# Kernel optimization log

Hardware: AMD Instinct MI355X
Metric: run time of the kernel (lower is better)

## Reference

```python
import jax, jax.numpy as jnp
import numpy as np

N, HW, A, G, C = 8, 4096, 9, 64, 80


def setup_inputs() -> dict:
    key = jax.random.key(0)
    k1, k2, k3, k4, k5, k6 = jax.random.split(key, 6)
    pred_boxes = jax.random.uniform(k1, (N, HW, A, 4), dtype=jnp.float32)  # (x, y, w, h) in [0,1)
    pred_o = jax.random.uniform(k2, (N, HW, A), dtype=jnp.float32)
    pred_scores = jax.random.normal(k3, (N, HW, A, C), dtype=jnp.float32)
    # valid xyxy ground-truth boxes with positive width/height
    xy = jax.random.uniform(k4, (N, G, 2), dtype=jnp.float32) * 0.7
    wh = 0.05 + jax.random.uniform(k5, (N, G, 2), dtype=jnp.float32) * 0.25
    gt_boxes = jnp.concatenate([xy, xy + wh], axis=-1)
    gt_labels = jax.random.randint(k6, (N, G), 0, C)
    return dict(pred_boxes=pred_boxes, pred_o=pred_o, pred_scores=pred_scores,
                gt_boxes=gt_boxes, gt_labels=gt_labels)


def _box_iou(b1, b2):
    # b1 [P,4], b2 [G,4] in xyxy -> [P,G]; same math as torchvision.ops.box_iou
    a1 = (b1[:, 2] - b1[:, 0]) * (b1[:, 3] - b1[:, 1])
    a2 = (b2[:, 2] - b2[:, 0]) * (b2[:, 3] - b2[:, 1])
    lt = jnp.maximum(b1[:, None, :2], b2[None, :, :2])
    rb = jnp.minimum(b1[:, None, 2:], b2[None, :, 2:])
    wh = jnp.clip(rb - lt, 0.0)
    inter = wh[..., 0] * wh[..., 1]
    return inter / (a1[:, None] + a2[None, :] - inter)


def _per_image(pb, po, ps, gb, gl):
    # pb [HW,A,4] already converted to xyxy, po [HW,A], ps [HW,A,C], gb [G,4], gl [G]
    iou = _box_iou(pb.reshape(-1, 4), gb).reshape(HW, A, G)
    cell_sel = iou.max(axis=(1, 2)) > 0.0                  # [HW] cells with any GT overlap
    anchor_sel = jnp.argmax(iou.max(axis=2), axis=1)       # [HW] best anchor per cell
    hw = jnp.arange(HW)
    sel_boxes = pb[hw, anchor_sel]                         # [HW,4]
    sel_o = po[hw, anchor_sel]                             # [HW]
    sel_scores = ps[hw, anchor_sel]                        # [HW,C]
    iou_sel = iou[hw, anchor_sel]                          # [HW,G]
    best_iou = iou_sel.max(axis=1)
    best_gt = jnp.argmax(iou_sel, axis=1)
    gt_b = gb[best_gt]                                     # [HW,4]
    gt_l = gl[best_gt]                                     # [HW]
    m = cell_sel.astype(pb.dtype)
    obj = jnp.sum(m * (sel_o - best_iou) ** 2)
    bbox = jnp.sum(m[:, None] * (sel_boxes[:, :2] - gt_b[:, :2]) ** 2)
    bbox += jnp.sum(m[:, None] * (jnp.sqrt(sel_boxes[:, 2:]) - jnp.sqrt(gt_b[:, 2:])) ** 2)
    ce = -jnp.take_along_axis(jax.nn.log_softmax(sel_scores, axis=-1), gt_l[:, None], axis=1)[:, 0]
    clf = jnp.sum(m * ce)
    # empty cells: penalize max objectness over anchors
    obj += 0.5 * jnp.sum((1.0 - m) * po.max(axis=1) ** 2)
    return obj, bbox, clf


def reference(pred_boxes, pred_o, pred_scores, gt_boxes, gt_labels):
    # (x,y,w,h) -> (x,y,x+w,y+h), as done in-place in the torch code
    pb = jnp.concatenate([pred_boxes[..., :2], pred_boxes[..., 2:] + pred_boxes[..., :2]], axis=-1)
    obj, bbox, clf = jax.vmap(_per_image)(pb, pred_o, pred_scores, gt_boxes, gt_labels)
    return jnp.stack([obj.sum(), bbox.sum(), clf.sum()])
```

## Files before the change

### kernel.cpp

```cpp
#include <hip/hip_runtime.h>
#include <math.h>

#define NIMG 8
#define HWC  4096
#define AA   9
#define GG   64
#define CC   80
#define CPB  64
#define BT   (CPB * AA)
#define NSLOT 32

__global__ __launch_bounds__(BT) void yolo_main(
    const float* __restrict__ pred_boxes,
    const float* __restrict__ pred_o,
    const float* __restrict__ pred_scores,
    const float* __restrict__ gt_boxes,
    const int*   __restrict__ gt_labels,
    float*       __restrict__ part)
{
    __shared__ float4 sbox[GG];
    __shared__ float  sarea[GG];
    __shared__ float  ssqx[GG];
    __shared__ float  ssqy[GG];
    __shared__ int    slab[GG];
    __shared__ float  Li[BT];
    __shared__ float  Ls[BT];
    __shared__ int    Lg[BT];
    __shared__ float4 Lbox[BT];
    __shared__ float  Lpo[BT];
    __shared__ int    Lsel[CPB];
    __shared__ int    Llbl[CPB];

    const int tid = threadIdx.x;
    const int n   = blockIdx.y;
    const int hw0 = blockIdx.x * CPB;

    if (tid < GG) {
        float4 gb = ((const float4*)gt_boxes)[n * GG + tid];
        sbox[tid]  = gb;
        sarea[tid] = (gb.z - gb.x) * (gb.w - gb.y);
        ssqx[tid]  = sqrtf(gb.z);
        ssqy[tid]  = sqrtf(gb.w);
        slab[tid]  = gt_labels[n * GG + tid];
    }
    __syncthreads();

    const int c    = tid / AA;
    const int a    = tid - c * AA;
    const int cell = hw0 + c;
    const int pidx = (n * HWC + cell) * AA + a;

    const float4 pb = ((const float4*)pred_boxes)[pidx];
    const float  po = pred_o[pidx];
    const float x1 = pb.x, y1 = pb.y;
    const float x2 = pb.x + pb.z, y2 = pb.y + pb.w;
    const float a1 = (x2 - x1) * (y2 - y1);

    float bi = -1.0f, bsv = 1.0f; int bg = 0;
    #pragma unroll 8
    for (int g = 0; g < GG; ++g) {
        float4 gb = sbox[g];
        float s  = a1 + sarea[g];
        float ix = fminf(x2, gb.z) - fmaxf(x1, gb.x);
        float iy = fminf(y2, gb.w) - fmaxf(y1, gb.y);
        float inter = fmaxf(ix, 0.0f) * fmaxf(iy, 0.0f);
        if (inter * bsv > bi * s) { bi = inter; bsv = s; bg = g; }
    }
    Li[tid]  = bi;
    Ls[tid]  = bsv;
    Lg[tid]  = bg;
    Lbox[tid] = make_float4(x1, y1, x2, y2);
    Lpo[tid] = po;
    __syncthreads();

    if (tid < CPB) {
        const int cc = tid;
        float bi2 = -1.0f, bs2 = 1.0f; int ba = 0;
        float pomax = -1e30f;
        #pragma unroll
        for (int aa2 = 0; aa2 < AA; ++aa2) {
            float ii = Li[cc * AA + aa2];
            float ss = Ls[cc * AA + aa2];
            if (ii * bs2 > bi2 * ss) { bi2 = ii; bs2 = ss; ba = aa2; }
            pomax = fmaxf(pomax, Lpo[cc * AA + aa2]);
        }
        float objv, bboxv = 0.0f;
        int selbase = -1, lbl = 0;
        if (bi2 > 0.0f) {
            float biou = bi2 / (bs2 - bi2);
            float4 sb  = Lbox[cc * AA + ba];
            int    g   = Lg[cc * AA + ba];
            float4 gb  = sbox[g];
            float  so  = Lpo[cc * AA + ba];
            float d = so - biou;
            objv = d * d;
            float dx = sb.x - gb.x, dy = sb.y - gb.y;
            float dz = sqrtf(sb.z) - ssqx[g];
            float dw = sqrtf(sb.w) - ssqy[g];
            bboxv = dx*dx + dy*dy + dz*dz + dw*dw;
            selbase = ((n * HWC + hw0 + cc) * AA + ba) * CC;
            lbl = slab[g];
        } else {
            objv = 0.5f * pomax * pomax;
        }
        Lsel[cc] = selbase;
        Llbl[cc] = lbl;
        float ov = objv, bv = bboxv;
        #pragma unroll
        for (int msk = 1; msk < 64; msk <<= 1) {
            ov += __shfl_xor(ov, msk);
            bv += __shfl_xor(bv, msk);
        }
        if (tid == 0) {
            int slot = blockIdx.x & (NSLOT - 1);
            atomicAdd(&part[0 * NSLOT + slot], ov);
            atomicAdd(&part[1 * NSLOT + slot], bv);
        }
    }
    __syncthreads();

    {
        const int sb = Lsel[c];
        float esum = 0.0f, selv = 0.0f;
        if (sb >= 0) {
            const int lbl = Llbl[c];
            #pragma unroll
            for (int i = 0; i < AA; ++i) {
                int e = a + AA * i;
                if (e < CC) {
                    float v = pred_scores[sb + e];
                    esum += __expf(v);
                    if (e == lbl) selv = v;
                }
            }
        }
        Li[tid] = esum;
        Ls[tid] = selv;
    }
    __syncthreads();

    if (tid < CPB) {
        float clfv = 0.0f;
        if (Lsel[tid] >= 0) {
            float S = 0.0f, sel = 0.0f;
            #pragma unroll
            for (int aa2 = 0; aa2 < AA; ++aa2) {
                S   += Li[tid * AA + aa2];
                sel += Ls[tid * AA + aa2];
            }
            clfv = __logf(S) - sel;
        }
        #pragma unroll
        for (int msk = 1; msk < 64; msk <<= 1) clfv += __shfl_xor(clfv, msk);
        if (tid == 0) {
            int slot = blockIdx.x & (NSLOT - 1);
            atomicAdd(&part[2 * NSLOT + slot], clfv);
        }
    }
}

__global__ void yolo_final(const float* __restrict__ part, float* __restrict__ out)
{
    int t = threadIdx.x;
    float v = (t < 3 * NSLOT) ? part[t] : 0.0f;
    #pragma unroll
    for (int msk = 1; msk < NSLOT; msk <<= 1) v += __shfl_xor(v, msk, NSLOT);
    if (t < 3 * NSLOT && (t & (NSLOT - 1)) == 0) out[t / NSLOT] = v;
}

extern "C" void kernel_launch(void* const* d_in, const int* in_sizes, int n_in,
                              void* d_out, int out_size, void* d_ws, size_t ws_size,
                              hipStream_t stream)
{
    const float* pred_boxes  = (const float*)d_in[0];
    const float* pred_o      = (const float*)d_in[1];
    const float* pred_scores = (const float*)d_in[2];
    const float* gt_boxes    = (const float*)d_in[3];
    const int*   gt_labels   = (const int*)d_in[4];
    float* part = (float*)d_ws;

    hipMemsetAsync(d_ws, 0, 3 * NSLOT * sizeof(float), stream);
    dim3 grid(HWC / CPB, NIMG);
    yolo_main<<<grid, BT, 0, stream>>>(pred_boxes, pred_o, pred_scores,
                                       gt_boxes, gt_labels, part);
    yolo_final<<<1, 128, 0, stream>>>(part, (float*)d_out);
}
```

Before: 146.6 us.

## Replace atomics and memset with per-block partials, vectorize score loads

Each block writes its objectness, bbox and classification partial sums to a dedicated workspace slot instead of atomically accumulating into 32 slots. This removes the memset launch and the atomic contention. The final kernel reduces all 512 partials with a 512-thread block. The IoU loop now reads GT boxes straight from global memory (cache-resident) with inline area computation, dropping the first block barrier, and class scores are loaded as float4.

```diff
diff --git a/kernel.cpp b/kernel.cpp
--- a/kernel.cpp
+++ b/kernel.cpp
@@ -8,7 +8,7 @@
 #define CC   80
 #define CPB  64
 #define BT   (CPB * AA)
-#define NSLOT 32
+#define NBLK (NIMG * (HWC / CPB))
 
 __global__ __launch_bounds__(BT) void yolo_main(
     const float* __restrict__ pred_boxes,
@@ -19,7 +19,6 @@
     float*       __restrict__ part)
 {
     __shared__ float4 sbox[GG];
-    __shared__ float  sarea[GG];
     __shared__ float  ssqx[GG];
     __shared__ float  ssqy[GG];
     __shared__ int    slab[GG];
@@ -37,13 +36,11 @@
 
     if (tid < GG) {
         float4 gb = ((const float4*)gt_boxes)[n * GG + tid];
-        sbox[tid]  = gb;
-        sarea[tid] = (gb.z - gb.x) * (gb.w - gb.y);
-        ssqx[tid]  = sqrtf(gb.z);
-        ssqy[tid]  = sqrtf(gb.w);
-        slab[tid]  = gt_labels[n * GG + tid];
-    }
-    __syncthreads();
+        sbox[tid] = gb;
+        ssqx[tid] = sqrtf(gb.z);
+        ssqy[tid] = sqrtf(gb.w);
+        slab[tid] = gt_labels[n * GG + tid];
+    }
 
     const int c    = tid / AA;
     const int a    = tid - c * AA;
@@ -56,15 +53,21 @@
     const float x2 = pb.x + pb.z, y2 = pb.y + pb.w;
     const float a1 = (x2 - x1) * (y2 - y1);
 
+    const float4* __restrict__ gbp = (const float4*)gt_boxes + n * GG;
+
     float bi = -1.0f, bsv = 1.0f; int bg = 0;
-    #pragma unroll 8
-    for (int g = 0; g < GG; ++g) {
-        float4 gb = sbox[g];
-        float s  = a1 + sarea[g];
-        float ix = fminf(x2, gb.z) - fmaxf(x1, gb.x);
-        float iy = fminf(y2, gb.w) - fmaxf(y1, gb.y);
-        float inter = fmaxf(ix, 0.0f) * fmaxf(iy, 0.0f);
-        if (inter * bsv > bi * s) { bi = inter; bsv = s; bg = g; }
+    #pragma unroll 1
+    for (int g0 = 0; g0 < GG; g0 += 8) {
+        #pragma unroll
+        for (int k = 0; k < 8; ++k) {
+            const float4 gb = gbp[g0 + k];
+            const float area = (gb.z - gb.x) * (gb.w - gb.y);
+            const float s  = a1 + area;
+            const float ix = fminf(x2, gb.z) - fmaxf(x1, gb.x);
+            const float iy = fminf(y2, gb.w) - fmaxf(y1, gb.y);
+            const float inter = fmaxf(ix, 0.0f) * fmaxf(iy, 0.0f);
+            if (inter * bsv > bi * s) { bi = inter; bsv = s; bg = g0 + k; }
+        }
     }
     Li[tid]  = bi;
     Ls[tid]  = bsv;
@@ -112,9 +115,9 @@
             bv += __shfl_xor(bv, msk);
         }
         if (tid == 0) {
-            int slot = blockIdx.x & (NSLOT - 1);
-            atomicAdd(&part[0 * NSLOT + slot], ov);
-            atomicAdd(&part[1 * NSLOT + slot], bv);
+            int slot = blockIdx.y * gridDim.x + blockIdx.x;
+            part[0 * NBLK + slot] = ov;
+            part[1 * NBLK + slot] = bv;
         }
     }
     __syncthreads();
@@ -125,12 +128,17 @@
         if (sb >= 0) {
             const int lbl = Llbl[c];
             #pragma unroll
-            for (int i = 0; i < AA; ++i) {
-                int e = a + AA * i;
-                if (e < CC) {
-                    float v = pred_scores[sb + e];
-                    esum += __expf(v);
-                    if (e == lbl) selv = v;
+            for (int i = 0; i < 3; ++i) {
+                int idx = a + AA * i;
+                if (idx < 20) {
+                    float4 v = *(const float4*)(pred_scores + sb + 4 * idx);
+                    esum += __expf(v.x) + __expf(v.y) + __expf(v.z) + __expf(v.w);
+                    int e0 = 4 * idx;
+                    if (lbl >= e0 && lbl < e0 + 4) {
+                        selv = (lbl == e0)     ? v.x :
+                               (lbl == e0 + 1) ? v.y :
+                               (lbl == e0 + 2) ? v.z : v.w;
+                    }
                 }
             }
         }
@@ -153,19 +161,36 @@
         #pragma unroll
         for (int msk = 1; msk < 64; msk <<= 1) clfv += __shfl_xor(clfv, msk);
         if (tid == 0) {
-            int slot = blockIdx.x & (NSLOT - 1);
-            atomicAdd(&part[2 * NSLOT + slot], clfv);
+            int slot = blockIdx.y * gridDim.x + blockIdx.x;
+            part[2 * NBLK + slot] = clfv;
         }
     }
 }
 
-__global__ void yolo_final(const float* __restrict__ part, float* __restrict__ out)
+__global__ __launch_bounds__(NBLK) void yolo_final(const float* __restrict__ part,
+                                                   float* __restrict__ out)
 {
-    int t = threadIdx.x;
-    float v = (t < 3 * NSLOT) ? part[t] : 0.0f;
+    __shared__ float s[3][NBLK / 64];
+    const int t = threadIdx.x;
+    float v0 = part[0 * NBLK + t];
+    float v1 = part[1 * NBLK + t];
+    float v2 = part[2 * NBLK + t];
     #pragma unroll
-    for (int msk = 1; msk < NSLOT; msk <<= 1) v += __shfl_xor(v, msk, NSLOT);
-    if (t < 3 * NSLOT && (t & (NSLOT - 1)) == 0) out[t / NSLOT] = v;
+    for (int msk = 1; msk < 64; msk <<= 1) {
+        v0 += __shfl_xor(v0, msk);
+        v1 += __shfl_xor(v1, msk);
+        v2 += __shfl_xor(v2, msk);
+    }
+    if ((t & 63) == 0) {
+        s[0][t >> 6] = v0; s[1][t >> 6] = v1; s[2][t >> 6] = v2;
+    }
+    __syncthreads();
+    if (t < 3) {
+        float acc = 0.0f;
+        #pragma unroll
+        for (int w = 0; w < NBLK / 64; ++w) acc += s[t][w];
+        out[t] = acc;
+    }
 }
 
 extern "C" void kernel_launch(void* const* d_in, const int* in_sizes, int n_in,
@@ -179,9 +204,8 @@
     const int*   gt_labels   = (const int*)d_in[4];
     float* part = (float*)d_ws;
 
-    hipMemsetAsync(d_ws, 0, 3 * NSLOT * sizeof(float), stream);
     dim3 grid(HWC / CPB, NIMG);
     yolo_main<<<grid, BT, 0, stream>>>(pred_boxes, pred_o, pred_scores,
                                        gt_boxes, gt_labels, part);
-    yolo_final<<<1, 128, 0, stream>>>(part, (float*)d_out);
+    yolo_final<<<1, NBLK, 0, stream>>>(part, (float*)d_out);
 }
```

After: 142.9 us. 1.03x faster.
